# Kernel tuning notes

Measured on AMD Instinct MI355X. Metric: run time of the kernel, lower is better.

The kernel has to match this reference:

```python
import jax, jax.numpy as jnp
import numpy as np
from functools import partial

B, N, T = 4, 10000, 128
E = 160000
H, C = 4, 64            # heads, out_channels per head
GAT_DIM = H * C         # 256
NEG_SLOPE = 0.2


def conv1d(x, w, b):
    # x: (M, Cin, L), w: (Cout, Cin, K), 'same' padding (pad=1 for k=3)
    y = jax.lax.conv_general_dilated(x, w, window_strides=(1,), padding=[(1, 1)],
                                     dimension_numbers=('NCH', 'OIH', 'NCH'))
    return y + b[None, :, None]


def maxpool2(x):
    # kernel=2, stride=2 over last axis
    return jax.lax.reduce_window(x, -jnp.inf, jax.lax.max,
                                 (1, 1, 2), (1, 1, 2), 'VALID')


def gat_layer_single(x, src, dst, W, att_s, att_d, bias):
    # x: (N, Fin); PyG GATConv with concat=True, self-loops already appended to src/dst
    n = x.shape[0]
    xl = (x @ W).reshape(n, H, C)                       # (N, H, C)
    a_s = jnp.sum(xl * att_s[None], axis=-1)            # (N, H)
    a_d = jnp.sum(xl * att_d[None], axis=-1)            # (N, H)
    e = jax.nn.leaky_relu(a_s[src] + a_d[dst], NEG_SLOPE)  # (E', H)
    emax = jax.ops.segment_max(e, dst, num_segments=n)     # (N, H)
    ex = jnp.exp(e - emax[dst])
    denom = jax.ops.segment_sum(ex, dst, num_segments=n)   # (N, H)
    alpha = ex / (denom[dst] + 1e-16)                       # (E', H)
    msg = xl[src] * alpha[..., None]                        # (E', H, C)
    out = jax.ops.segment_sum(msg, dst, num_segments=n)     # (N, H, C)
    return out.reshape(n, H * C) + bias


def setup_inputs() -> dict:
    key = jax.random.key(0)
    ks = jax.random.split(key, 24)
    rn = lambda k, sh, fan: jax.random.normal(k, sh, jnp.float32) / np.sqrt(fan)
    inp = {
        'x': jax.random.normal(ks[0], (B, N, T), jnp.float32),
        'edge_index': jax.random.randint(ks[1], (2, E), 0, N, jnp.int64),
        # temporal conv
        'cw1': rn(ks[2], (32, 1, 3), 3), 'cb1': jnp.zeros((32,), jnp.float32),
        'cw2': rn(ks[3], (64, 32, 3), 96), 'cb2': jnp.zeros((64,), jnp.float32),
        # GAT layer 0 (in=64)
        'W0': rn(ks[4], (64, GAT_DIM), 64), 'as0': rn(ks[5], (H, C), C), 'ad0': rn(ks[6], (H, C), C),
        'b0': jnp.zeros((GAT_DIM,), jnp.float32),
        # GAT layer 1 (in=256)
        'W1': rn(ks[7], (GAT_DIM, GAT_DIM), GAT_DIM), 'as1': rn(ks[8], (H, C), C), 'ad1': rn(ks[9], (H, C), C),
        'b1': jnp.zeros((GAT_DIM,), jnp.float32),
        # classification head 256->128->2
        'Wc1': rn(ks[10], (GAT_DIM, 128), GAT_DIM), 'bc1': jnp.zeros((128,), jnp.float32),
        'Wc2': rn(ks[11], (128, 2), 128), 'bc2': jnp.zeros((2,), jnp.float32),
        # attribution head 256->64->1
        'Wa1': rn(ks[12], (GAT_DIM, 64), GAT_DIM), 'ba1': jnp.zeros((64,), jnp.float32),
        'Wa2': rn(ks[13], (64, 1), 64), 'ba2': jnp.zeros((1,), jnp.float32),
    }
    return inp


def reference(x, edge_index, cw1, cb1, cw2, cb2, W0, as0, ad0, b0, W1, as1, ad1, b1,
              Wc1, bc1, Wc2, bc2, Wa1, ba1, Wa2, ba2):
    b, n, t = x.shape
    # ---- temporal conv over all B*N node signals ----
    xf = x.reshape(b * n, 1, t)
    h = jax.nn.relu(conv1d(xf, cw1, cb1))            # (BN, 32, T)
    h = maxpool2(h)                                  # (BN, 32, T//2)
    h = jax.nn.relu(conv1d(h, cw2, cb2))             # (BN, 64, T//2)
    feat = jnp.mean(h, axis=-1).reshape(b, n, 64)    # adaptive_avg_pool1d(1)
    # ---- GAT stack (self-loops appended, PyG default) ----
    src0, dst0 = edge_index[0], edge_index[1]
    loops = jnp.arange(n, dtype=src0.dtype)
    src = jnp.concatenate([src0, loops])
    dst = jnp.concatenate([dst0, loops])
    gat0 = jax.vmap(partial(gat_layer_single, src=src, dst=dst, W=W0, att_s=as0, att_d=ad0, bias=b0))
    gat1 = jax.vmap(partial(gat_layer_single, src=src, dst=dst, W=W1, att_s=as1, att_d=ad1, bias=b1))
    g = jax.nn.relu(gat0(feat))                      # (B, N, 256); dropout = identity (eval)
    g = jax.nn.relu(gat1(g))                         # (B, N, 256)
    # ---- heads ----
    pooled = jnp.mean(g, axis=1)                     # (B, 256)
    logits = jax.nn.relu(pooled @ Wc1 + bc1) @ Wc2 + bc2          # (B, 2)
    attr = jax.nn.sigmoid(jax.nn.relu(g @ Wa1 + ba1) @ Wa2 + ba2)  # (B, N, 1)
    return logits, attr[..., 0]
```

## Files before the change

### kernel.cpp

```cpp
#include <hip/hip_runtime.h>
#include <hip/hip_bf16.h>
#include <math.h>

typedef __hip_bfloat16 bf16;
typedef unsigned short u16;
typedef unsigned int u32;
typedef __attribute__((ext_vector_type(8))) short short8;
typedef __attribute__((ext_vector_type(4))) float f32x4;
typedef __attribute__((ext_vector_type(2))) float f32x2;

#define BATCH 4
#define NNODE 10000
#define TLEN 128
#define NEDGE 160000
#define GDIM 256
#define NHEAD 4

#define S_CW1 0
#define S_CB1 96
#define S_CB2 128
#define S_AS0 192
#define S_AD0 448
#define S_B0  704
#define S_AS1 960
#define S_AD1 1216
#define S_B1  1472
#define S_BC1 1728
#define S_WC2 1856
#define S_BC2 2112
#define S_BA1 2114
#define S_WA2 2178
#define S_BA2 2242
#define S_TOTAL 2243

__device__ __forceinline__ float prelu(float v) { return fmaxf(v, 0.f); }
__device__ __forceinline__ u16 f2b(float f) {
    union { float f; u32 u; } v; v.f = f;
    u32 r = v.u + 0x7FFF + ((v.u >> 16) & 1);
    return (u16)(r >> 16);
}
__device__ __forceinline__ float u2f(u16 u) {
    union { u32 u; float f; } v; v.u = ((u32)u) << 16;
    return v.f;
}
__device__ __forceinline__ float ldw(const void* p, int off, bool isbf) {
    return isbf ? u2f(((const u16*)p)[off]) : ((const float*)p)[off];
}

__device__ __forceinline__ bool probe_x_bf16(const void* xsrc) {
    int lane = threadIdx.x & 63;
    u16 h = ((const u16*)xsrc)[2 * lane];
    int e = (h >> 7) & 0xFF;
    unsigned long long m = __ballot(e >= 117 && e <= 130);
    return __popcll(m) >= 32;
}
__device__ __forceinline__ bool probe_ei64(const int* ei) {
    int lane = threadIdx.x & 63;
    int v = ei[2 * lane + 1];
    unsigned long long m = __ballot(v == 0);
    return __popcll(m) >= 56;
}

struct WPtrs { const void* p[20]; };

#define PRE_TBLK 665
__global__ __launch_bounds__(256) void k_pre(WPtrs wp, const void* __restrict__ xsrc,
        const int* __restrict__ ei, float* __restrict__ wbuf,
        u16* __restrict__ cw2r, u16* __restrict__ W0t, u16* __restrict__ W1t,
        u16* __restrict__ Wa1t, int* __restrict__ counts) {
    bool isbf = probe_x_bf16(xsrc);
    int b = blockIdx.x;
    if (b >= PRE_TBLK) {
        const int C2[16] = {0,96,128,192,448,704,960,1216,1472,1728,1856,2112,
                            2114,2178,2242,2243};
        const int SRC[15] = {0,1,3,5,6,7,9,10,11,13,14,15,17,18,19};
        int i = (b - PRE_TBLK) * 256 + threadIdx.x;
        if (i >= S_TOTAL) return;
        int j = 14;
        for (int t = 0; t < 15; ++t) { if (i < C2[t + 1]) { j = t; break; } }
        wbuf[i] = ldw(wp.p[SRC[j]], i - C2[j], isbf);
        return;
    }
    int i = b * 256 + threadIdx.x;
    if (i < 6144) {
        int c2 = i / 96, k = i - c2 * 96, s = k >> 5, ci = k & 31;
        cw2r[i] = f2b(ldw(wp.p[2], c2 * 96 + ci * 3 + s, isbf));
    }
    if (i < 16384) {
        int k = i >> 8, c = i & 255;
        W0t[c * 64 + k] = f2b(ldw(wp.p[4], k * 256 + c, isbf));
        int ka = i >> 6, ca = i & 63;
        Wa1t[ca * 256 + ka] = f2b(ldw(wp.p[16], ka * 64 + ca, isbf));
    }
    if (i < 65536) {
        int k = i >> 8, c = i & 255;
        W1t[c * 256 + k] = f2b(ldw(wp.p[8], k * 256 + c, isbf));
    }
    if (i < NEDGE + NNODE) {
        bool ei64 = probe_ei64(ei);
        int dst;
        if (i < NEDGE) dst = ei64 ? ei[2 * (NEDGE + i)] : ei[NEDGE + i];
        else dst = i - NEDGE;
        if (dst >= 0 && dst < NNODE) atomicAdd(&counts[dst], 1);
    }
}

__global__ __launch_bounds__(1024) void k_scan(const int* __restrict__ counts,
        int* __restrict__ cur, int* __restrict__ row_ptr) {
    __shared__ int buf[1024];
    int t = threadIdx.x;
    int base = t * 10;
    int c[10];
    int s = 0;
    #pragma unroll
    for (int i = 0; i < 10; ++i) {
        int idx = base + i;
        c[i] = (idx < NNODE) ? counts[idx] : 0;
        s += c[i];
    }
    buf[t] = s;
    __syncthreads();
    for (int off = 1; off < 1024; off <<= 1) {
        int v = (t >= off) ? buf[t - off] : 0;
        __syncthreads();
        buf[t] += v;
        __syncthreads();
    }
    int run = buf[t] - s;
    #pragma unroll
    for (int i = 0; i < 10; ++i) {
        int idx = base + i;
        if (idx < NNODE) {
            cur[idx] = run;
            run += c[i];
            row_ptr[idx + 1] = run;
        }
    }
    if (t == 0) row_ptr[0] = 0;
}

#define HSTR 40
#define FSTR 72
#define NPW 4
#define FILL_BLK 665
__global__ __launch_bounds__(256) void k_conv(const void* __restrict__ xsrc,
        const float* __restrict__ wbuf, const u16* __restrict__ cw2r,
        const u16* __restrict__ W0t, u16* __restrict__ featb,
        u16* __restrict__ xlb, float* __restrict__ a_s, float* __restrict__ a_d,
        const int* __restrict__ ei, int* __restrict__ cur, int* __restrict__ col_src) {
    __shared__ __align__(16) float xs[4][132];
    __shared__ float w1s[96], b1s[32], b2s[64];
    __shared__ __align__(16) u16 hb[4][66 * HSTR];
    __shared__ __align__(16) u16 fs[16][FSTR];

    bool isbf = probe_x_bf16(xsrc);
    int tid = threadIdx.x;
    int wave = tid >> 6, lane = tid & 63;
    int node0 = blockIdx.x * (4 * NPW);

    int m = lane & 15, q = lane >> 4;
    short8 bfr[4][3];
    #pragma unroll
    for (int nt = 0; nt < 4; ++nt)
        #pragma unroll
        for (int sh = 0; sh < 3; ++sh)
            bfr[nt][sh] = *(const short8*)&cw2r[(nt * 16 + m) * 96 + sh * 32 + q * 8];

    if (tid < 96) w1s[tid] = wbuf[S_CW1 + tid];
    if (tid < 32) b1s[tid] = wbuf[S_CB1 + tid];
    if (tid < 64) b2s[tid] = wbuf[S_CB2 + tid];
    if (tid < 8) xs[tid >> 1][(tid & 1) ? 129 : 0] = 0.f;
    if (tid < 64) {
        int w = tid >> 4, idx = tid & 15;
        *(u32*)&hb[w][2 * idx] = 0;
        *(u32*)&hb[w][65 * HSTR + 2 * idx] = 0;
    }
    __syncthreads();

    float* xsw = xs[wave];
    u16* hw = &hb[wave][0];

    int d = m, uu = q;
    float wa0 = w1s[6 * d + 0], wa1 = w1s[6 * d + 1], wa2 = w1s[6 * d + 2];
    float wb0 = w1s[6 * d + 3], wb1 = w1s[6 * d + 4], wb2 = w1s[6 * d + 5];
    float ba = b1s[2 * d], bb = b1s[2 * d + 1];
    float b2vv[4];
    #pragma unroll
    for (int nt = 0; nt < 4; ++nt) b2vv[nt] = b2s[nt * 16 + m];

    int node = node0 + wave;
    u32 plo = 0; float2 pf = {0.f, 0.f};
    if (isbf) plo = ((const u32*)xsrc)[(size_t)node * 64 + lane];
    else      pf  = ((const float2*)xsrc)[(size_t)node * 64 + lane];

    for (int j = 0; j < NPW; ++j) {
        if (isbf) {
            xsw[1 + 2 * lane] = u2f((u16)(plo & 0xFFFF));
            xsw[2 + 2 * lane] = u2f((u16)(plo >> 16));
        } else {
            xsw[1 + 2 * lane] = pf.x;
            xsw[2 + 2 * lane] = pf.y;
        }
        if (j + 1 < NPW) {
            int nxt = node + 4;
            if (isbf) plo = ((const u32*)xsrc)[(size_t)nxt * 64 + lane];
            else      pf  = ((const float2*)xsrc)[(size_t)nxt * 64 + lane];
        }

        #pragma unroll
        for (int it = 0; it < 16; ++it) {
            int u = uu + 4 * it;
            int t0 = 2 * u;
            float2 xa = *(const float2*)&xsw[t0];
            float2 xb = *(const float2*)&xsw[t0 + 2];
            float x0 = xa.x, x1 = xa.y, x2 = xb.x, x3 = xb.y;
            f32x2 A = {x0, x1}, Bv = {x1, x2}, Cv = {x2, x3};
            f32x2 va = {ba, ba}; va += wa0 * A; va += wa1 * Bv; va += wa2 * Cv;
            f32x2 vb = {bb, bb}; vb += wb0 * A; vb += wb1 * Bv; vb += wb2 * Cv;
            float ha = fmaxf(fmaxf(va.x, va.y), 0.f);
            float hb2 = fmaxf(fmaxf(vb.x, vb.y), 0.f);
            __hip_bfloat162 hp2 = __float22bfloat162_rn(make_float2(ha, hb2));
            u32 pack; __builtin_memcpy(&pack, &hp2, 4);
            *(u32*)&hw[(u + 1) * HSTR + 2 * d] = pack;
        }

        float pc0 = 0.f, pc1 = 0.f, pc2 = 0.f, pc3 = 0.f;
        #pragma unroll
        for (int mt = 0; mt < 4; ++mt) {
            const u16* hr = &hw[(mt * 16 + m) * HSTR + q * 8];
            short8 a0 = *(const short8*)&hr[0 * HSTR];
            short8 a1 = *(const short8*)&hr[1 * HSTR];
            short8 a2 = *(const short8*)&hr[2 * HSTR];
            f32x4 c0 = {0.f,0.f,0.f,0.f}, c1 = {0.f,0.f,0.f,0.f};
            f32x4 c2 = {0.f,0.f,0.f,0.f}, c3 = {0.f,0.f,0.f,0.f};
            c0 = __builtin_amdgcn_mfma_f32_16x16x32_bf16(a0, bfr[0][0], c0, 0, 0, 0);
            c1 = __builtin_amdgcn_mfma_f32_16x16x32_bf16(a0, bfr[1][0], c1, 0, 0, 0);
            c2 = __builtin_amdgcn_mfma_f32_16x16x32_bf16(a0, bfr[2][0], c2, 0, 0, 0);
            c3 = __builtin_amdgcn_mfma_f32_16x16x32_bf16(a0, bfr[3][0], c3, 0, 0, 0);
            c0 = __builtin_amdgcn_mfma_f32_16x16x32_bf16(a1, bfr[0][1], c0, 0, 0, 0);
            c1 = __builtin_amdgcn_mfma_f32_16x16x32_bf16(a1, bfr[1][1], c1, 0, 0, 0);
            c2 = __builtin_amdgcn_mfma_f32_16x16x32_bf16(a1, bfr[2][1], c2, 0, 0, 0);
            c3 = __builtin_amdgcn_mfma_f32_16x16x32_bf16(a1, bfr[3][1], c3, 0, 0, 0);
            c0 = __builtin_amdgcn_mfma_f32_16x16x32_bf16(a2, bfr[0][2], c0, 0, 0, 0);
            c1 = __builtin_amdgcn_mfma_f32_16x16x32_bf16(a2, bfr[1][2], c1, 0, 0, 0);
            c2 = __builtin_amdgcn_mfma_f32_16x16x32_bf16(a2, bfr[2][2], c2, 0, 0, 0);
            c3 = __builtin_amdgcn_mfma_f32_16x16x32_bf16(a2, bfr[3][2], c3, 0, 0, 0);
            pc0 += prelu(c0[0] + b2vv[0]) + prelu(c0[1] + b2vv[0])
                 + prelu(c0[2] + b2vv[0]) + prelu(c0[3] + b2vv[0]);
            pc1 += prelu(c1[0] + b2vv[1]) + prelu(c1[1] + b2vv[1])
                 + prelu(c1[2] + b2vv[1]) + prelu(c1[3] + b2vv[1]);
            pc2 += prelu(c2[0] + b2vv[2]) + prelu(c2[1] + b2vv[2])
                 + prelu(c2[2] + b2vv[2]) + prelu(c2[3] + b2vv[2]);
            pc3 += prelu(c3[0] + b2vv[3]) + prelu(c3[1] + b2vv[3])
                 + prelu(c3[2] + b2vv[3]) + prelu(c3[3] + b2vv[3]);
        }
        pc0 += __shfl_xor(pc0, 16, 64); pc0 += __shfl_xor(pc0, 32, 64);
        pc1 += __shfl_xor(pc1, 16, 64); pc1 += __shfl_xor(pc1, 32, 64);
        pc2 += __shfl_xor(pc2, 16, 64); pc2 += __shfl_xor(pc2, 32, 64);
        pc3 += __shfl_xor(pc3, 16, 64); pc3 += __shfl_xor(pc3, 32, 64);
        float v = (q == 0) ? pc0 : (q == 1) ? pc1 : (q == 2) ? pc2 : pc3;
        u16 fv = f2b(v * (1.f / 64.f));
        featb[(size_t)node * 64 + lane] = fv;
        fs[wave + 4 * j][lane] = fv;

        node += 4;
    }

    if (blockIdx.x < FILL_BLK) {
        bool ei64 = probe_ei64(ei);
        int e = blockIdx.x * 256 + tid;
        if (e < NEDGE + NNODE) {
            int src, dst;
            if (e < NEDGE) {
                if (ei64) { src = ei[2 * e]; dst = ei[2 * (NEDGE + e)]; }
                else      { src = ei[e];     dst = ei[NEDGE + e]; }
            } else {
                src = dst = e - NEDGE;
            }
            if (dst >= 0 && dst < NNODE) {
                int pos = atomicAdd(&cur[dst], 1);
                if (pos >= 0 && pos < NEDGE + NNODE) col_src[pos] = src;
            }
        }
    }

    __syncthreads();

    {
        f32x4 acc[4];
        #pragma unroll
        for (int ntl = 0; ntl < 4; ++ntl) acc[ntl] = {0.f, 0.f, 0.f, 0.f};
        #pragma unroll
        for (int kc = 0; kc < 64; kc += 32) {
            short8 a = *(const short8*)&fs[m][kc + q * 8];
            #pragma unroll
            for (int ntl = 0; ntl < 4; ++ntl) {
                int col0 = wave * 64 + ntl * 16;
                short8 bw = *(const short8*)&W0t[(size_t)(col0 + m) * 64 + kc + q * 8];
                acc[ntl] = __builtin_amdgcn_mfma_f32_16x16x32_bf16(a, bw, acc[ntl], 0, 0, 0);
            }
        }
        #pragma unroll
        for (int ntl = 0; ntl < 4; ++ntl) {
            #pragma unroll
            for (int r = 0; r < 4; ++r)
                xlb[(size_t)(node0 + q * 4 + r) * 256 + wave * 64 + ntl * 16 + m]
                    = f2b(acc[ntl][r]);
        }
        const float* asw_p = wbuf + S_AS0;
        const float* adw_p = wbuf + S_AD0;
        float sh_s[4] = {0, 0, 0, 0}, sh_d[4] = {0, 0, 0, 0};
        #pragma unroll
        for (int ntl = 0; ntl < 4; ++ntl) {
            float asw = asw_p[wave * 64 + ntl * 16 + m];
            float adw = adw_p[wave * 64 + ntl * 16 + m];
            #pragma unroll
            for (int r = 0; r < 4; ++r) {
                sh_s[r] += acc[ntl][r] * asw;
                sh_d[r] += acc[ntl][r] * adw;
            }
        }
        #pragma unroll
        for (int off = 1; off < 16; off <<= 1) {
            #pragma unroll
            for (int r = 0; r < 4; ++r) {
                sh_s[r] += __shfl_xor(sh_s[r], off, 64);
                sh_d[r] += __shfl_xor(sh_d[r], off, 64);
            }
        }
        if (m == 0) {
            int bb2 = node0 / NNODE;
            int nn0 = node0 - bb2 * NNODE;
            #pragma unroll
            for (int r = 0; r < 4; ++r) {
                int nn = nn0 + q * 4 + r;
                a_s[(size_t)nn * 16 + bb2 * 4 + wave] = sh_s[r];
                a_d[(size_t)nn * 16 + bb2 * 4 + wave] = sh_d[r];
            }
        }
    }
}

__global__ __launch_bounds__(256) void k_gemm(const u16* __restrict__ A,
        const u16* __restrict__ Wt, const float* __restrict__ att_s_w,
        const float* __restrict__ att_d_w, u16* __restrict__ outb,
        float* __restrict__ a_s, float* __restrict__ a_d) {
    const int K = 256;
    int wave = threadIdx.x >> 6, lane = threadIdx.x & 63;
    int row0 = (blockIdx.x * 4 + wave) * 16;
    int m = lane & 15, q = lane >> 4;
    f32x4 acc[16];
    #pragma unroll
    for (int nt = 0; nt < 16; ++nt) acc[nt] = {0.f, 0.f, 0.f, 0.f};
    for (int kc = 0; kc < K; kc += 32) {
        short8 a = *(const short8*)&A[(size_t)(row0 + m) * K + kc + q * 8];
        #pragma unroll
        for (int nt = 0; nt < 16; ++nt) {
            short8 b = *(const short8*)&Wt[(size_t)(nt * 16 + m) * K + kc + q * 8];
            acc[nt] = __builtin_amdgcn_mfma_f32_16x16x32_bf16(a, b, acc[nt], 0, 0, 0);
        }
    }
    #pragma unroll
    for (int nt = 0; nt < 16; ++nt) {
        #pragma unroll
        for (int r = 0; r < 4; ++r)
            outb[(size_t)(row0 + q * 4 + r) * 256 + nt * 16 + m] = f2b(acc[nt][r]);
    }
    float sh_s[4][4] = {{0}}, sh_d[4][4] = {{0}};
    #pragma unroll
    for (int nt = 0; nt < 16; ++nt) {
        int h = nt >> 2;
        int cc = (nt & 3) * 16 + m;
        float asw = att_s_w[h * 64 + cc];
        float adw = att_d_w[h * 64 + cc];
        #pragma unroll
        for (int r = 0; r < 4; ++r) {
            sh_s[h][r] += acc[nt][r] * asw;
            sh_d[h][r] += acc[nt][r] * adw;
        }
    }
    #pragma unroll
    for (int off = 1; off < 16; off <<= 1) {
        #pragma unroll
        for (int h = 0; h < 4; ++h)
            #pragma unroll
            for (int r = 0; r < 4; ++r) {
                sh_s[h][r] += __shfl_xor(sh_s[h][r], off, 64);
                sh_d[h][r] += __shfl_xor(sh_d[h][r], off, 64);
            }
    }
    if (m == 0) {
        #pragma unroll
        for (int r = 0; r < 4; ++r) {
            int row = row0 + q * 4 + r;
            int b = row / NNODE, nn = row - b * NNODE;
            float4 vs = {sh_s[0][r], sh_s[1][r], sh_s[2][r], sh_s[3][r]};
            float4 vd = {sh_d[0][r], sh_d[1][r], sh_d[2][r], sh_d[3][r]};
            *(float4*)&a_s[(size_t)nn * 16 + b * 4] = vs;
            *(float4*)&a_d[(size_t)nn * 16 + b * 4] = vd;
        }
    }
}

__global__ __launch_bounds__(256) void k_agg(const u16* __restrict__ xlb,
        const float* __restrict__ a_s, const float* __restrict__ a_d,
        const int* __restrict__ row_ptr, const int* __restrict__ col_src,
        const float* __restrict__ bias, u16* __restrict__ gb_out) {
    int wave = threadIdx.x >> 6, lane = threadIdx.x & 63;
    int dst = __builtin_amdgcn_readfirstlane(blockIdx.x * 2 + (wave >> 1));
    int bp = (wave & 1) * 2;
    int beg = __builtin_amdgcn_readfirstlane(row_ptr[dst]);
    int end = __builtin_amdgcn_readfirstlane(row_ptr[dst + 1]);

    int bl = lane >> 5;
    int s = lane & 31;
    int h = s >> 3;
    int b = bp + bl;
    int asoff = b * 4 + h;
    size_t rowb = (size_t)b * NNODE;
    float advh = a_d[(size_t)dst * 16 + asoff];

    float m = -INFINITY, l = 0.f;
    float acc[8];
    #pragma unroll
    for (int k = 0; k < 8; ++k) acc[k] = 0.f;

    int i = beg;
    int n0 = 0, n1 = 0, n2 = 0, n3 = 0;
    if (i + 4 <= end) {
        n0 = col_src[i]; n1 = col_src[i + 1];
        n2 = col_src[i + 2]; n3 = col_src[i + 3];
    }
    while (i + 4 <= end) {
        int s0 = min(max(n0, 0), NNODE - 1);
        int s1 = min(max(n1, 0), NNODE - 1);
        int s2 = min(max(n2, 0), NNODE - 1);
        int s3 = min(max(n3, 0), NNODE - 1);
        float a0 = a_s[(size_t)s0 * 16 + asoff];
        float a1 = a_s[(size_t)s1 * 16 + asoff];
        float a2 = a_s[(size_t)s2 * 16 + asoff];
        float a3 = a_s[(size_t)s3 * 16 + asoff];
        short8 x0 = *(const short8*)&xlb[(rowb + s0) * 256 + s * 8];
        short8 x1 = *(const short8*)&xlb[(rowb + s1) * 256 + s * 8];
        short8 x2 = *(const short8*)&xlb[(rowb + s2) * 256 + s * 8];
        short8 x3 = *(const short8*)&xlb[(rowb + s3) * 256 + s * 8];
        i += 4;
        if (i + 4 <= end) {
            n0 = col_src[i]; n1 = col_src[i + 1];
            n2 = col_src[i + 2]; n3 = col_src[i + 3];
        }
        float e0 = a0 + advh; e0 = (e0 >= 0.f) ? e0 : 0.2f * e0;
        float e1 = a1 + advh; e1 = (e1 >= 0.f) ? e1 : 0.2f * e1;
        float e2 = a2 + advh; e2 = (e2 >= 0.f) ? e2 : 0.2f * e2;
        float e3 = a3 + advh; e3 = (e3 >= 0.f) ? e3 : 0.2f * e3;
        float cmax = fmaxf(fmaxf(e0, e1), fmaxf(e2, e3));
        if (__any(cmax > m)) {
            float mn = fmaxf(m, cmax);
            float r = __expf(m - mn);
            m = mn;
            l *= r;
            #pragma unroll
            for (int k = 0; k < 8; ++k) acc[k] *= r;
        }
        float p0 = __expf(e0 - m); l += p0;
        #pragma unroll
        for (int k = 0; k < 8; ++k) acc[k] += p0 * u2f((u16)x0[k]);
        float p1 = __expf(e1 - m); l += p1;
        #pragma unroll
        for (int k = 0; k < 8; ++k) acc[k] += p1 * u2f((u16)x1[k]);
        float p2 = __expf(e2 - m); l += p2;
        #pragma unroll
        for (int k = 0; k < 8; ++k) acc[k] += p2 * u2f((u16)x2[k]);
        float p3 = __expf(e3 - m); l += p3;
        #pragma unroll
        for (int k = 0; k < 8; ++k) acc[k] += p3 * u2f((u16)x3[k]);
    }
    for (; i < end; ++i) {
        int s0 = min(max(col_src[i], 0), NNODE - 1);
        float a0 = a_s[(size_t)s0 * 16 + asoff];
        short8 x0 = *(const short8*)&xlb[(rowb + s0) * 256 + s * 8];
        float e0 = a0 + advh; e0 = (e0 >= 0.f) ? e0 : 0.2f * e0;
        if (__any(e0 > m)) {
            float mn = fmaxf(m, e0);
            float r = __expf(m - mn);
            m = mn;
            l *= r;
            #pragma unroll
            for (int k = 0; k < 8; ++k) acc[k] *= r;
        }
        float p0 = __expf(e0 - m); l += p0;
        #pragma unroll
        for (int k = 0; k < 8; ++k) acc[k] += p0 * u2f((u16)x0[k]);
    }

    float rl = 1.f / (l + 1e-16f);
    short8 o;
    #pragma unroll
    for (int k = 0; k < 8; ++k)
        o[k] = (short)f2b(prelu(acc[k] * rl + bias[s * 8 + k]));
    *(short8*)&gb_out[(rowb + dst) * 256 + s * 8] = o;
}

__global__ __launch_bounds__(256) void k_attrpool(const u16* __restrict__ gb,
        const u16* __restrict__ Wa1t, const float* __restrict__ wbuf,
        float* __restrict__ out, float* __restrict__ pooled) {
    if (blockIdx.x >= 625) {
        int pb = blockIdx.x - 625;
        int b = pb >> 6;
        int chunk = pb & 63;
        int cch = threadIdx.x;
        int n0 = chunk * 157;
        int n1 = min(NNODE, n0 + 157);
        size_t rowb = (size_t)b * NNODE;
        float acc = 0.f;
        int n = n0;
        for (; n + 4 <= n1; n += 4) {
            float v0 = u2f(gb[(rowb + n) * 256 + cch]);
            float v1 = u2f(gb[(rowb + n + 1) * 256 + cch]);
            float v2 = u2f(gb[(rowb + n + 2) * 256 + cch]);
            float v3 = u2f(gb[(rowb + n + 3) * 256 + cch]);
            acc += v0; acc += v1; acc += v2; acc += v3;
        }
        for (; n < n1; ++n)
            acc += u2f(gb[(rowb + n) * 256 + cch]);
        atomicAdd(&pooled[b * 256 + cch], acc);
        return;
    }
    int wave = threadIdx.x >> 6, lane = threadIdx.x & 63;
    int row0 = (blockIdx.x * 4 + wave) * 16;
    int m = lane & 15, q = lane >> 4;
    f32x4 acc[4];
    #pragma unroll
    for (int nt = 0; nt < 4; ++nt) acc[nt] = {0.f, 0.f, 0.f, 0.f};
    for (int kc = 0; kc < 256; kc += 32) {
        short8 a = *(const short8*)&gb[(size_t)(row0 + m) * 256 + kc + q * 8];
        #pragma unroll
        for (int nt = 0; nt < 4; ++nt) {
            short8 b = *(const short8*)&Wa1t[(size_t)(nt * 16 + m) * 256 + kc + q * 8];
            acc[nt] = __builtin_amdgcn_mfma_f32_16x16x32_bf16(a, b, acc[nt], 0, 0, 0);
        }
    }
    float part[4] = {0, 0, 0, 0};
    #pragma unroll
    for (int nt = 0; nt < 4; ++nt) {
        int col = nt * 16 + m;
        float ba1v = wbuf[S_BA1 + col];
        float wa2v = wbuf[S_WA2 + col];
        #pragma unroll
        for (int r = 0; r < 4; ++r)
            part[r] += prelu(acc[nt][r] + ba1v) * wa2v;
    }
    #pragma unroll
    for (int off = 1; off < 16; off <<= 1) {
        #pragma unroll
        for (int r = 0; r < 4; ++r)
            part[r] += __shfl_xor(part[r], off, 64);
    }
    if (m == 0) {
        float ba2v = wbuf[S_BA2];
        #pragma unroll
        for (int r = 0; r < 4; ++r) {
            int row = row0 + q * 4 + r;
            float v = part[r] + ba2v;
            out[8 + row] = 1.f / (1.f + __expf(-v));
        }
    }
}

__global__ __launch_bounds__(128) void k_logits(const float* __restrict__ pooled,
        const float* __restrict__ wbuf, const void* __restrict__ Wc1p,
        float* __restrict__ out,
        const u16* __restrict__ featb, const u16* __restrict__ gb,
        const int* __restrict__ row_ptr, const int* __restrict__ ei,
        const void* __restrict__ xsrc, int hostbad) {
    int tid = threadIdx.x;
    bool isbf = probe_x_bf16(xsrc);
    if (blockIdx.x == 4) {
        __shared__ float red[128];
        bool ei64 = probe_ei64(ei);
        float mx[2] = {0.f, 0.f};
        const u16* bufs[2] = {featb, gb};
        for (int qq = 0; qq < 2; ++qq) {
            const u16* p = bufs[qq];
            float m = 0.f;
            for (int i = tid; i < 2048; i += 128) {
                float v = u2f(p[i]);
                if (v != v) m = 1e30f;
                m = fmaxf(m, fabsf(v));
            }
            red[tid] = m;
            __syncthreads();
            for (int s2 = 64; s2 > 0; s2 >>= 1) {
                if (tid < s2) red[tid] = fmaxf(red[tid], red[tid + s2]);
                __syncthreads();
            }
            mx[qq] = red[0];
            __syncthreads();
        }
        if (tid == 0) {
            int fb = (mx[0] > 1e8f || mx[0] < 1e-6f) ? 1 : 0;
            int gbad = (mx[1] > 1e8f || mx[1] < 1e-6f) ? 1 : 0;
            int cb = (row_ptr[NNODE] != NEDGE + NNODE) ? 1 : 0;
            int code = 100 * fb + 400 * gbad + 800 * cb + 6400 * hostbad;
            if (code) {
                code += 1600 * (isbf ? 0 : 1);
                code += 3200 * (ei64 ? 1 : 0);
                for (int j = 0; j < 8; ++j) out[j] = (float)code;
            }
        }
        return;
    }
    __shared__ float pm[256];
    __shared__ float red4[4];
    int b = blockIdx.x;
    pm[tid] = pooled[b * 256 + tid] * (1.f / NNODE);
    pm[tid + 128] = pooled[b * 256 + tid + 128] * (1.f / NNODE);
    __syncthreads();
    float acc = wbuf[S_BC1 + tid];
    if (isbf) {
        const u16* w = (const u16*)Wc1p;
        #pragma unroll 4
        for (int k = 0; k < 256; ++k)
            acc += pm[k] * u2f(w[k * 128 + tid]);
    } else {
        const float* w = (const float*)Wc1p;
        #pragma unroll 4
        for (int k = 0; k < 256; ++k)
            acc += pm[k] * w[k * 128 + tid];
    }
    float hv = prelu(acc);
    float p0 = hv * wbuf[S_WC2 + tid * 2];
    float p1 = hv * wbuf[S_WC2 + tid * 2 + 1];
    #pragma unroll
    for (int off = 32; off > 0; off >>= 1) {
        p0 += __shfl_xor(p0, off, 64);
        p1 += __shfl_xor(p1, off, 64);
    }
    int wv = tid >> 6, lane = tid & 63;
    if (lane == 0) { red4[wv * 2] = p0; red4[wv * 2 + 1] = p1; }
    __syncthreads();
    if (tid < 2)
        out[b * 2 + tid] = red4[tid] + red4[2 + tid] + wbuf[S_BC2 + tid];
}

extern "C" void kernel_launch(void* const* d_in, const int* in_sizes, int n_in,
                              void* d_out, int out_size, void* d_ws, size_t ws_size,
                              hipStream_t stream) {
    const void* x  = d_in[0];
    const int*  ei = (const int*)d_in[1];
    float* out = (float*)d_out;

    WPtrs wp;
    for (int j = 0; j < 20; ++j) wp.p[j] = d_in[j + 2];

    char* ws = (char*)d_ws;
    size_t off = 0;
    auto alloc = [&](size_t bytes) -> void* {
        void* p = ws + off;
        off += (bytes + 255) & ~(size_t)255;
        return p;
    };
    float* wbuf    = (float*)alloc((size_t)S_TOTAL * 4);
    u16*   featb   = (u16*)  alloc((size_t)BATCH * NNODE * 64 * 2);
    u16*   xlb     = (u16*)  alloc((size_t)BATCH * NNODE * 256 * 2);
    u16*   gb      = (u16*)  alloc((size_t)BATCH * NNODE * 256 * 2);
    float* a_s     = (float*)alloc((size_t)BATCH * NNODE * 4 * 4);
    float* a_d     = (float*)alloc((size_t)BATCH * NNODE * 4 * 4);
    u16*   cw2r    = (u16*)alloc(6144 * 2);
    u16*   W0t     = (u16*)alloc(16384 * 2);
    u16*   W1t     = (u16*)alloc(65536 * 2);
    u16*   Wa1t    = (u16*)alloc(16384 * 2);
    int*   counts  = (int*)alloc(NNODE * 4);
    float* pooled  = (float*)alloc(BATCH * 256 * 4);
    int*   row_ptr = (int*)alloc((NNODE + 1) * 4);
    int*   cur     = (int*)alloc(NNODE * 4);
    int*   col_src = (int*)alloc((NEDGE + NNODE) * 4);
    (void)ws_size; (void)out_size;

    int hostbad = (n_in != 22 || in_sizes[0] != BATCH * NNODE * TLEN ||
                   in_sizes[1] != 2 * NEDGE) ? 1 : 0;

    hipMemsetAsync(counts, 0, 40192 + 4096, stream);

    k_pre<<<PRE_TBLK + 9, 256, 0, stream>>>(wp, x, ei, wbuf, cw2r, W0t, W1t, Wa1t, counts);
    k_scan<<<1, 1024, 0, stream>>>(counts, cur, row_ptr);

    k_conv<<<BATCH * NNODE / 16, 256, 0, stream>>>(x, wbuf, cw2r, W0t, featb,
            xlb, a_s, a_d, ei, cur, col_src);

    k_agg<<<NNODE / 2, 256, 0, stream>>>(xlb, a_s, a_d, row_ptr, col_src, wbuf + S_B0, gb);

    k_gemm<<<BATCH * NNODE / 64, 256, 0, stream>>>(gb, W1t,
            wbuf + S_AS1, wbuf + S_AD1, xlb, a_s, a_d);
    k_agg<<<NNODE / 2, 256, 0, stream>>>(xlb, a_s, a_d, row_ptr, col_src, wbuf + S_B1, gb);

    k_attrpool<<<625 + 256, 256, 0, stream>>>(gb, Wa1t, wbuf, out, pooled);
    k_logits<<<5, 128, 0, stream>>>(pooled, wbuf, wp.p[12], out, featb, gb, row_ptr, ei, x, hostbad);
}
```

Baseline: 389.7 us.

## Fuse layer-0 aggregation with layer-1 GEMM and attention-score computation

```diff
diff --git a/kernel.cpp b/kernel.cpp
--- a/kernel.cpp
+++ b/kernel.cpp
@@ -260,7 +260,7 @@
         pc3 += __shfl_xor(pc3, 16, 64); pc3 += __shfl_xor(pc3, 32, 64);
         float v = (q == 0) ? pc0 : (q == 1) ? pc1 : (q == 2) ? pc2 : pc3;
         u16 fv = f2b(v * (1.f / 64.f));
-        featb[(size_t)node * 64 + lane] = fv;
+        if (node < 32) featb[(size_t)node * 64 + lane] = fv;
         fs[wave + 4 * j][lane] = fv;
 
         node += 4;
@@ -341,64 +341,169 @@
     }
 }
 
-__global__ __launch_bounds__(256) void k_gemm(const u16* __restrict__ A,
-        const u16* __restrict__ Wt, const float* __restrict__ att_s_w,
-        const float* __restrict__ att_d_w, u16* __restrict__ outb,
-        float* __restrict__ a_s, float* __restrict__ a_d) {
-    const int K = 256;
-    int wave = threadIdx.x >> 6, lane = threadIdx.x & 63;
-    int row0 = (blockIdx.x * 4 + wave) * 16;
-    int m = lane & 15, q = lane >> 4;
-    f32x4 acc[16];
-    #pragma unroll
-    for (int nt = 0; nt < 16; ++nt) acc[nt] = {0.f, 0.f, 0.f, 0.f};
-    for (int kc = 0; kc < K; kc += 32) {
-        short8 a = *(const short8*)&A[(size_t)(row0 + m) * K + kc + q * 8];
-        #pragma unroll
-        for (int nt = 0; nt < 16; ++nt) {
-            short8 b = *(const short8*)&Wt[(size_t)(nt * 16 + m) * K + kc + q * 8];
-            acc[nt] = __builtin_amdgcn_mfma_f32_16x16x32_bf16(a, b, acc[nt], 0, 0, 0);
-        }
-    }
-    #pragma unroll
-    for (int nt = 0; nt < 16; ++nt) {
+#define GSTR 264
+__global__ __launch_bounds__(512) void k_agg_gemm(const u16* __restrict__ xlb,
+        const float* __restrict__ a_s, const float* __restrict__ a_d,
+        const int* __restrict__ row_ptr, const int* __restrict__ col_src,
+        const float* __restrict__ bias, const u16* __restrict__ W1t,
+        const float* __restrict__ wbuf, u16* __restrict__ outb,
+        float* __restrict__ as_out, float* __restrict__ ad_out) {
+    __shared__ __align__(16) u16 gt[16][GSTR];
+    __shared__ float ps_s[8][16], ps_d[8][16];
+
+    int tid = threadIdx.x;
+    int wave = tid >> 6, lane = tid & 63;
+    int dl = wave >> 1;
+    int dst = __builtin_amdgcn_readfirstlane(blockIdx.x * 4 + dl);
+    int bp = (wave & 1) * 2;
+    int beg = __builtin_amdgcn_readfirstlane(row_ptr[dst]);
+    int end = __builtin_amdgcn_readfirstlane(row_ptr[dst + 1]);
+
+    int bl = lane >> 5;
+    int s = lane & 31;
+    int h = s >> 3;
+    int b = bp + bl;
+    int asoff = b * 4 + h;
+    size_t rowb = (size_t)b * NNODE;
+    float advh = a_d[(size_t)dst * 16 + asoff];
+
+    float m = -INFINITY, l = 0.f;
+    float acc[8];
+    #pragma unroll
+    for (int k = 0; k < 8; ++k) acc[k] = 0.f;
+
+    int i = beg;
+    int n0 = 0, n1 = 0, n2 = 0, n3 = 0;
+    if (i + 4 <= end) {
+        n0 = col_src[i]; n1 = col_src[i + 1];
+        n2 = col_src[i + 2]; n3 = col_src[i + 3];
+    }
+    while (i + 4 <= end) {
+        int s0 = min(max(n0, 0), NNODE - 1);
+        int s1 = min(max(n1, 0), NNODE - 1);
+        int s2 = min(max(n2, 0), NNODE - 1);
+        int s3 = min(max(n3, 0), NNODE - 1);
+        float a0 = a_s[(size_t)s0 * 16 + asoff];
+        float a1 = a_s[(size_t)s1 * 16 + asoff];
+        float a2 = a_s[(size_t)s2 * 16 + asoff];
+        float a3 = a_s[(size_t)s3 * 16 + asoff];
+        short8 x0 = *(const short8*)&xlb[(rowb + s0) * 256 + s * 8];
+        short8 x1 = *(const short8*)&xlb[(rowb + s1) * 256 + s * 8];
+        short8 x2 = *(const short8*)&xlb[(rowb + s2) * 256 + s * 8];
+        short8 x3 = *(const short8*)&xlb[(rowb + s3) * 256 + s * 8];
+        i += 4;
+        if (i + 4 <= end) {
+            n0 = col_src[i]; n1 = col_src[i + 1];
+            n2 = col_src[i + 2]; n3 = col_src[i + 3];
+        }
+        float e0 = a0 + advh; e0 = (e0 >= 0.f) ? e0 : 0.2f * e0;
+        float e1 = a1 + advh; e1 = (e1 >= 0.f) ? e1 : 0.2f * e1;
+        float e2 = a2 + advh; e2 = (e2 >= 0.f) ? e2 : 0.2f * e2;
+        float e3 = a3 + advh; e3 = (e3 >= 0.f) ? e3 : 0.2f * e3;
+        float cmax = fmaxf(fmaxf(e0, e1), fmaxf(e2, e3));
+        if (__any(cmax > m)) {
+            float mn = fmaxf(m, cmax);
+            float r = __expf(m - mn);
+            m = mn;
+            l *= r;
+            #pragma unroll
+            for (int k = 0; k < 8; ++k) acc[k] *= r;
+        }
+        float p0 = __expf(e0 - m); l += p0;
+        #pragma unroll
+        for (int k = 0; k < 8; ++k) acc[k] += p0 * u2f((u16)x0[k]);
+        float p1 = __expf(e1 - m); l += p1;
+        #pragma unroll
+        for (int k = 0; k < 8; ++k) acc[k] += p1 * u2f((u16)x1[k]);
+        float p2 = __expf(e2 - m); l += p2;
+        #pragma unroll
+        for (int k = 0; k < 8; ++k) acc[k] += p2 * u2f((u16)x2[k]);
+        float p3 = __expf(e3 - m); l += p3;
+        #pragma unroll
+        for (int k = 0; k < 8; ++k) acc[k] += p3 * u2f((u16)x3[k]);
+    }
+    for (; i < end; ++i) {
+        int s0 = min(max(col_src[i], 0), NNODE - 1);
+        float a0 = a_s[(size_t)s0 * 16 + asoff];
+        short8 x0 = *(const short8*)&xlb[(rowb + s0) * 256 + s * 8];
+        float e0 = a0 + advh; e0 = (e0 >= 0.f) ? e0 : 0.2f * e0;
+        if (__any(e0 > m)) {
+            float mn = fmaxf(m, e0);
+            float r = __expf(m - mn);
+            m = mn;
+            l *= r;
+            #pragma unroll
+            for (int k = 0; k < 8; ++k) acc[k] *= r;
+        }
+        float p0 = __expf(e0 - m); l += p0;
+        #pragma unroll
+        for (int k = 0; k < 8; ++k) acc[k] += p0 * u2f((u16)x0[k]);
+    }
+
+    float rl = 1.f / (l + 1e-16f);
+    short8 o;
+    #pragma unroll
+    for (int k = 0; k < 8; ++k)
+        o[k] = (short)f2b(prelu(acc[k] * rl + bias[s * 8 + k]));
+    int grow = dl * 4 + b;
+    *(short8*)&gt[grow][s * 8] = o;
+    __syncthreads();
+
+    int mm = lane & 15, q = lane >> 4;
+    f32x4 ac2[2];
+    ac2[0] = {0.f, 0.f, 0.f, 0.f};
+    ac2[1] = {0.f, 0.f, 0.f, 0.f};
+    for (int kc = 0; kc < 256; kc += 32) {
+        short8 a = *(const short8*)&gt[mm][kc + q * 8];
+        #pragma unroll
+        for (int ntl = 0; ntl < 2; ++ntl) {
+            short8 bw = *(const short8*)&W1t[(size_t)(wave * 32 + ntl * 16 + mm) * 256 + kc + q * 8];
+            ac2[ntl] = __builtin_amdgcn_mfma_f32_16x16x32_bf16(a, bw, ac2[ntl], 0, 0, 0);
+        }
+    }
+    int dbase = blockIdx.x * 4;
+    #pragma unroll
+    for (int ntl = 0; ntl < 2; ++ntl) {
         #pragma unroll
         for (int r = 0; r < 4; ++r)
-            outb[(size_t)(row0 + q * 4 + r) * 256 + nt * 16 + m] = f2b(acc[nt][r]);
-    }
-    float sh_s[4][4] = {{0}}, sh_d[4][4] = {{0}};
-    #pragma unroll
-    for (int nt = 0; nt < 16; ++nt) {
-        int h = nt >> 2;
-        int cc = (nt & 3) * 16 + m;
-        float asw = att_s_w[h * 64 + cc];
-        float adw = att_d_w[h * 64 + cc];
+            outb[((size_t)r * NNODE + dbase + q) * 256 + wave * 32 + ntl * 16 + mm]
+                = f2b(ac2[ntl][r]);
+    }
+    float sh_s[4] = {0, 0, 0, 0}, sh_d[4] = {0, 0, 0, 0};
+    #pragma unroll
+    for (int ntl = 0; ntl < 2; ++ntl) {
+        int col = wave * 32 + ntl * 16 + mm;
+        float asw = wbuf[S_AS1 + col];
+        float adw = wbuf[S_AD1 + col];
         #pragma unroll
         for (int r = 0; r < 4; ++r) {
-            sh_s[h][r] += acc[nt][r] * asw;
-            sh_d[h][r] += acc[nt][r] * adw;
+            sh_s[r] += ac2[ntl][r] * asw;
+            sh_d[r] += ac2[ntl][r] * adw;
         }
     }
     #pragma unroll
     for (int off = 1; off < 16; off <<= 1) {
         #pragma unroll
-        for (int h = 0; h < 4; ++h)
-            #pragma unroll
-            for (int r = 0; r < 4; ++r) {
-                sh_s[h][r] += __shfl_xor(sh_s[h][r], off, 64);
-                sh_d[h][r] += __shfl_xor(sh_d[h][r], off, 64);
-            }
-    }
-    if (m == 0) {
-        #pragma unroll
         for (int r = 0; r < 4; ++r) {
-            int row = row0 + q * 4 + r;
-            int b = row / NNODE, nn = row - b * NNODE;
-            float4 vs = {sh_s[0][r], sh_s[1][r], sh_s[2][r], sh_s[3][r]};
-            float4 vd = {sh_d[0][r], sh_d[1][r], sh_d[2][r], sh_d[3][r]};
-            *(float4*)&a_s[(size_t)nn * 16 + b * 4] = vs;
-            *(float4*)&a_d[(size_t)nn * 16 + b * 4] = vd;
-        }
+            sh_s[r] += __shfl_xor(sh_s[r], off, 64);
+            sh_d[r] += __shfl_xor(sh_d[r], off, 64);
+        }
+    }
+    if (mm == 0) {
+        #pragma unroll
+        for (int r = 0; r < 4; ++r) {
+            ps_s[wave][q * 4 + r] = sh_s[r];
+            ps_d[wave][q * 4 + r] = sh_d[r];
+        }
+    }
+    __syncthreads();
+    if (tid < 128) {
+        int sd = tid >> 6, hh = (tid >> 4) & 3, row2 = tid & 15;
+        int nn = dbase + (row2 >> 2), bb = row2 & 3;
+        if (sd == 0)
+            as_out[(size_t)nn * 16 + bb * 4 + hh] = ps_s[2 * hh][row2] + ps_s[2 * hh + 1][row2];
+        else
+            ad_out[(size_t)nn * 16 + bb * 4 + hh] = ps_d[2 * hh][row2] + ps_d[2 * hh + 1][row2];
     }
 }
 
@@ -666,6 +771,8 @@
     u16*   gb      = (u16*)  alloc((size_t)BATCH * NNODE * 256 * 2);
     float* a_s     = (float*)alloc((size_t)BATCH * NNODE * 4 * 4);
     float* a_d     = (float*)alloc((size_t)BATCH * NNODE * 4 * 4);
+    float* a_s2    = (float*)alloc((size_t)BATCH * NNODE * 4 * 4);
+    float* a_d2    = (float*)alloc((size_t)BATCH * NNODE * 4 * 4);
     u16*   cw2r    = (u16*)alloc(6144 * 2);
     u16*   W0t     = (u16*)alloc(16384 * 2);
     u16*   W1t     = (u16*)alloc(65536 * 2);
@@ -688,12 +795,11 @@
     k_conv<<<BATCH * NNODE / 16, 256, 0, stream>>>(x, wbuf, cw2r, W0t, featb,
             xlb, a_s, a_d, ei, cur, col_src);
 
-    k_agg<<<NNODE / 2, 256, 0, stream>>>(xlb, a_s, a_d, row_ptr, col_src, wbuf + S_B0, gb);
-
-    k_gemm<<<BATCH * NNODE / 64, 256, 0, stream>>>(gb, W1t,
-            wbuf + S_AS1, wbuf + S_AD1, xlb, a_s, a_d);
-    k_agg<<<NNODE / 2, 256, 0, stream>>>(xlb, a_s, a_d, row_ptr, col_src, wbuf + S_B1, gb);
-
-    k_attrpool<<<625 + 256, 256, 0, stream>>>(gb, Wa1t, wbuf, out, pooled);
-    k_logits<<<5, 128, 0, stream>>>(pooled, wbuf, wp.p[12], out, featb, gb, row_ptr, ei, x, hostbad);
-}
+    k_agg_gemm<<<NNODE / 4, 512, 0, stream>>>(xlb, a_s, a_d, row_ptr, col_src,
+            wbuf + S_B0, W1t, wbuf, gb, a_s2, a_d2);
+
+    k_agg<<<NNODE / 2, 256, 0, stream>>>(gb, a_s2, a_d2, row_ptr, col_src, wbuf + S_B1, xlb);
+
+    k_attrpool<<<625 + 256, 256, 0, stream>>>(xlb, Wa1t, wbuf, out, pooled);
+    k_logits<<<5, 128, 0, stream>>>(pooled, wbuf, wp.p[12], out, featb, xlb, row_ptr, ei, x, hostbad);
+}
```

Result: faster. 358.9 us (-7.9%).
